# Kernel tuning notes

Hardware: AMD Instinct MI355X
Metric: run time of the kernel (lower is better)

The kernel has to match this reference:

```python
import jax, jax.numpy as jnp
import numpy as np

N, K, BINS, DIM = 32, 16, 100, 2
LAST_TIME = 1.0
PRIOR_LAMBDA = 1.0e5
T_INIT, T_LAST = 1.0, 2.0
JITTER = 1e-5
EPS = 1e-12


def _b_kernel(t1, t2, ls, x0_c):
    """RBF kernel between train bin centers t2 (rows) and query times t1 (cols),
    with an independent x0 block prepended (block_diag). Returns (len(t2)+1, len(t1)+1)."""
    tm = t1[None, :] - t2[:, None]                      # (P, M)
    ker = jnp.exp(-0.5 * (tm / ls[0]) ** 2)
    P, M = ker.shape
    top = jnp.concatenate([x0_c ** 2, jnp.zeros((M,), ker.dtype)])[None, :]   # (1, M+1)
    bot = jnp.concatenate([jnp.zeros((P, 1), ker.dtype), ker], axis=1)        # (P, M+1)
    return jnp.concatenate([top, bot], axis=0)


def setup_inputs() -> dict:
    key = jax.random.key(0)
    ks = jax.random.split(key, 7)
    return {
        "x0": jax.random.normal(ks[0], (N, DIM), jnp.float32),
        "v": 0.1 * jax.random.normal(ks[1], (BINS, N, DIM), jnp.float32),
        "beta": jax.random.normal(ks[2], (N,), jnp.float32),
        "prior_sigma": 0.1 + 0.9 * jax.random.uniform(ks[3], (1,), jnp.float32),
        "prior_B_x0_c": 0.5 + jax.random.uniform(ks[4], (1,), jnp.float32),
        "prior_B_ls": 0.1 + 0.4 * jax.random.uniform(ks[5], (1,), jnp.float32),
        "prior_C_Q": 0.1 * jax.random.normal(ks[6], (N, K), jnp.float32),
        "sample_size": 100,
    }


def reference(x0, v, beta, prior_sigma, prior_B_x0_c, prior_B_ls, prior_C_Q, sample_size):
    bounds = jnp.linspace(0.0, LAST_TIME, BINS + 1)
    centers = 0.5 * (bounds[1:] + bounds[:-1])           # (BINS,)

    # ---- __compute_inv_train_cov (Woodbury via Kronecker factors) ----
    Bk = _b_kernel(centers, centers, prior_B_ls, prior_B_x0_c)          # (BINS+1, BINS+1)
    B_factor = jnp.linalg.cholesky(Bk + JITTER * jnp.eye(BINS + 1, dtype=Bk.dtype))
    C_factor = prior_C_Q                                                 # (N, K)
    D_factor = jnp.eye(DIM, dtype=x0.dtype)

    sigma_sq = jnp.clip(prior_sigma, 5.0 / BINS, None)[0] ** 2
    sigma_sq_inv = 1.0 / sigma_sq
    lambda_sq = PRIOR_LAMBDA ** 2
    reduced_dim = K * (BINS + 1) * DIM
    final_dim = N * (BINS + 1) * DIM

    R = jnp.eye(reduced_dim, dtype=x0.dtype) + sigma_sq_inv * jnp.kron(
        B_factor.T @ B_factor, jnp.kron(C_factor.T @ C_factor, D_factor.T @ D_factor))
    R_factor = jnp.linalg.cholesky(R)
    R_factor_inv = jnp.linalg.inv(R_factor).T
    K_factor = jnp.kron(B_factor, jnp.kron(C_factor, D_factor))          # (final_dim, reduced_dim)
    f = sigma_sq_inv * (K_factor @ R_factor_inv)
    inv_train_cov = (1.0 / lambda_sq) * (sigma_sq_inv * jnp.eye(final_dim, dtype=x0.dtype) - f @ f.T)

    # ---- get_v_pred / get_x_pred (noise term omitted for determinism) ----
    ts = jnp.linspace(T_INIT, T_LAST, sample_size)[:-1]                  # (T,)
    delta_t = ts[1] - ts[0]
    T = sample_size - 1

    B_cross = _b_kernel(ts, centers, prior_B_ls, prior_B_x0_c)[:, 1:]    # (BINS+1, T)
    CCt = C_factor @ C_factor.T                                          # (N, N)
    test_train_cov = lambda_sq * jnp.kron(B_cross, jnp.kron(CCt, D_factor @ D_factor.T))  # (final_dim, T*N*DIM)

    x0v = jnp.concatenate([x0.reshape(-1), v.reshape(-1)])               # (final_dim,)
    pred_v = ((test_train_cov.T @ inv_train_cov) @ x0v).reshape(T, N, DIM)

    bin_width = LAST_TIME / BINS
    x_last = x0 + bin_width * v.sum(axis=0)                              # (N, DIM)
    xt = x_last[None] + (ts - LAST_TIME)[:, None, None] * pred_v         # (T, N, DIM)

    # ---- intensity integral ----
    beta_mat = beta[:, None] + beta[None, :]                             # (N, N)
    sq = jnp.sum((xt[:, :, None, :] - xt[:, None, :, :]) ** 2, axis=-1)  # (T, N, N)
    dist = jnp.sqrt(jnp.maximum(sq, EPS))
    lambda_pred = jnp.sum(jnp.exp(beta_mat[None] - dist), axis=0) * delta_t
    return lambda_pred
```

## Files before the change

kernel.cpp:

```cpp
#include <hip/hip_runtime.h>
#include <math.h>

#define NBINS 100
#define NN    32
#define KD    16
#define NT    99

#define OFF_H   0
#define OFF_QT  3200
#define OFF_XL  3712

template<int CTRL>
__device__ __forceinline__ float fmov_dpp(float x) {
  return __int_as_float(
      __builtin_amdgcn_update_dpp(0, __float_as_int(x), CTRL, 0xf, 0xf, true));
}
__device__ __forceinline__ float frdlane(float x, int lane) {
  return __int_as_float(__builtin_amdgcn_readlane(__float_as_int(x), lane));
}
__device__ __forceinline__ float fshup(float x, float c0, int lane) {
  float v = fmov_dpp<0x111>(x);
  float x15 = frdlane(x, 15), x31 = frdlane(x, 31), x47 = frdlane(x, 47);
  v = (lane == 0)  ? c0  : v;
  v = (lane == 16) ? x15 : v;
  v = (lane == 32) ? x31 : v;
  v = (lane == 48) ? x47 : v;
  return v;
}
__device__ __forceinline__ float frdpos(float lo, float hi, int k) {
  return (k < 64) ? frdlane(lo, k) : frdlane(hi, k - 64);
}
__device__ __forceinline__ float frcp(float x) {
  float r = __builtin_amdgcn_rcpf(x);
  return r * (2.0f - x * r);
}

#define RD_LO(lo, hi, idx)  frdlane(lo, idx)
#define RD_MIX(lo, hi, idx) frdpos(lo, hi, ((idx) <= 99 ? (idx) : 99))

#define FWD_STEP(RD)                                                     \
  {                                                                      \
    float iuk = frcp(uk);                                                \
    Lrow[l * 101 + k] = u_lo * iuk;                                      \
    if (hiv) Lrow[ahi * 101 + k] = u_hi * iuk;                           \
    float dk = P * iuk * iuk;                                            \
    sdl = (l == k)   ? dk : sdl;                                         \
    sdh = (ahi == k) ? dk : sdh;                                         \
    float a0 = r0k * iuk, a1 = r1k * iuk;                                \
    float r0k1 = RD(r0_lo, r0_hi, k + 1);                                \
    float r1k1 = RD(r1_lo, r1_hi, k + 1);                                \
    float uk2  = RD(u_lo, u_hi, k + 2);                                  \
    float vk3  = RD(v_lo, v_hi, k + 3);                                  \
    if (l > k)   { r0_lo -= a0 * u_lo; r1_lo -= a1 * u_lo; }             \
    if (ahi > k) { r0_hi -= a0 * u_hi; r1_hi -= a1 * u_hi; }             \
    r0k = r0k1 - a0 * uk1;                                               \
    r1k = r1k1 - a1 * uk1;                                               \
    float g = vk1 * iuk;                                                 \
    float u63 = frdlane(u_lo, 63);                                       \
    float u1_lo = fshup(u_lo, 0.0f, l);                                  \
    float u1_hi = fshup(u_hi, u63, l);                                   \
    u_lo = u1_lo - g * v_lo;  u_hi = u1_hi - g * v_hi;                   \
    v_lo = v_lo - g * u1_lo;  v_hi = v_hi - g * u1_hi;                   \
    P *= (1.0f - g * g);                                                 \
    float uk_n  = uk  - g * vk1;                                         \
    float uk1_n = uk1 - g * vk2;                                         \
    float vk1_n = vk2 - g * uk1;                                         \
    float vk2_n = vk3 - g * uk2;                                         \
    uk = uk_n; uk1 = uk1_n; vk1 = vk1_n; vk2 = vk2_n;                    \
  }

__global__ __launch_bounds__(64) void k1_all(
    const float* __restrict__ x0, const float* __restrict__ v_in,
    const float* __restrict__ sigma_in, const float* __restrict__ ls_in,
    const float* __restrict__ Cq, float* __restrict__ ws)
{
  extern __shared__ float fsm[];
  float* Lrow  = fsm;
  float* vT    = Lrow + 100 * 101;
  float* QTl   = vT + 64 * 101;
  __shared__ float A[16 * 17], Vv[16 * 17];
  __shared__ float csC[16], csS[16];
  __shared__ float CqS[NN * KD];

  const int l = threadIdx.x;
  const int j = blockIdx.x;
  const int r = l >> 2, c0 = l & 3;
  const float ls = ls_in[0];
  const float i2 = -0.5f / (ls * ls);
  float sig = fmaxf(sigma_in[0], 0.05f);
  const double sinvd = 1.0 / ((double)sig * (double)sig);
  const float sinvf = (float)sinvd;
  const int ahi = 64 + l;
  const bool hiv = (ahi < 100);

  for (int p = 0; p < NBINS; ++p) vT[l * 101 + p] = v_in[p * 64 + l];
  for (int e = l; e < NN * KD; e += 64) CqS[e] = Cq[e];

  if (j == 0) {
    float acc = 0.f;
    for (int p = 0; p < NBINS; ++p) acc += vT[l * 101 + p];
    ws[OFF_XL + l] = x0[l] + 0.01f * acc;
  }

  #pragma unroll
  for (int k = 0; k < 4; ++k) {
    int ci = c0 + 4 * k;
    float acc = 0.f;
    for (int n = 0; n < NN; ++n)
      acc += CqS[n * 16 + r] * CqS[n * 16 + ci];
    A[r * 17 + ci] = acc;
    Vv[r * 17 + ci] = (r == ci) ? 1.0f : 0.0f;
  }

  for (int sweep = 0; sweep < 4; ++sweep)
  for (int m = 1; m <= 15; ++m) {
    const int hb = 31 - __clz(m);
    const int lowm = (1 << hb) - 1;
    if (l < 8) {
      int p = ((l & ~lowm) << 1) | (l & lowm), q = p ^ m;
      float app = A[p * 17 + p], aqq = A[q * 17 + q], apq = A[p * 17 + q];
      float c = 1.0f, s = 0.0f;
      if (fabsf(apq) > 1e-30f) {
        float th = (aqq - app) * 0.5f * __builtin_amdgcn_rcpf(apq);
        float t_ = __builtin_amdgcn_rcpf(fabsf(th) + sqrtf(th * th + 1.0f));
        t_ = (th >= 0.0f) ? t_ : -t_;
        c = __builtin_amdgcn_rsqf(t_ * t_ + 1.0f);
        s = t_ * c;
      }
      csC[p] = c; csS[p] = -s;
      csC[q] = c; csS[q] = s;
    }
    const int rh = r ^ m;
    float ar = csC[r], br = csS[r];
    float nA[4], nV[4];
    #pragma unroll
    for (int k = 0; k < 4; ++k) {
      int ci = c0 + 4 * k, ch = ci ^ m;
      float ac = csC[ci], bc = csS[ci];
      float a_rc = A[r * 17 + ci],  a_hc = A[rh * 17 + ci];
      float a_rh = A[r * 17 + ch],  a_hh = A[rh * 17 + ch];
      float v_rc = Vv[r * 17 + ci], v_rh = Vv[r * 17 + ch];
      nA[k] = ac * (ar * a_rc + br * a_hc) + bc * (ar * a_rh + br * a_hh);
      nV[k] = ac * v_rc + bc * v_rh;
    }
    #pragma unroll
    for (int k = 0; k < 4; ++k) {
      int ci = c0 + 4 * k;
      A[r * 17 + ci] = nA[k];
      Vv[r * 17 + ci] = nV[k];
    }
  }

  float muj = A[j * 17 + j];
  if (muj < 0.f) muj = 0.f;
  const float c = (float)(sinvd * (double)muj);
  if (j == 0) {
    for (int e = l; e < 512; e += 64) {
      int jq = e >> 5, n = e & 31;
      float acc = 0.f;
      for (int k2 = 0; k2 < 16; ++k2)
        acc += CqS[n * 16 + k2] * Vv[k2 * 17 + jq];
      QTl[e] = acc;
      ws[OFF_QT + e] = acc;
    }
  } else if (l < 32) {
    float acc = 0.f;
    for (int k2 = 0; k2 < 16; ++k2)
      acc += CqS[l * 16 + k2] * Vv[k2 * 17 + j];
    QTl[j * 32 + l] = acc;
  }

  float s0l = 0.f, s1l = 0.f, s0h = 0.f, s1h = 0.f;
  for (int n = 0; n < NN; ++n) {
    float qv = QTl[j * 32 + n];
    s0l += qv * vT[(2 * n) * 101 + l];
    s1l += qv * vT[(2 * n + 1) * 101 + l];
    if (hiv) {
      s0h += qv * vT[(2 * n) * 101 + ahi];
      s1h += qv * vT[(2 * n + 1) * 101 + ahi];
    }
  }

  const float m0  = 1.0f + c * (1.0f + 1e-5f);
  const float im0 = frcp(m0);
  float gl = expf((0.01f * (float)l) * (0.01f * (float)l) * i2);
  float gh = expf((0.01f * (float)ahi) * (0.01f * (float)ahi) * i2);
  float u_lo = (l == 0) ? 1.0f : c * gl * im0;
  float u_hi = hiv ? c * gh * im0 : 0.0f;
  float v_lo = (l == 0) ? 0.0f : u_lo;
  float v_hi = u_hi;
  float r0_lo = s0l * im0, r1_lo = s1l * im0;
  float r0_hi = hiv ? s0h * im0 : 0.0f;
  float r1_hi = hiv ? s1h * im0 : 0.0f;
  float P = 1.0f;
  float sdl = 0.f, sdh = 0.f;

  float uk  = frdlane(u_lo, 0);
  float uk1 = frdlane(u_lo, 1);
  float vk1 = frdlane(v_lo, 1);
  float vk2 = frdlane(v_lo, 2);
  float r0k = frdlane(r0_lo, 0);
  float r1k = frdlane(r1_lo, 0);

  for (int k = 0; k < 60; ++k)  FWD_STEP(RD_LO)
  for (int k = 60; k < 99; ++k) FWD_STEP(RD_MIX)
  {
    const int k = 99;
    float iuk = frcp(uk);
    Lrow[l * 101 + k] = u_lo * iuk;
    if (hiv) Lrow[ahi * 101 + k] = u_hi * iuk;
    float dk = P * iuk * iuk;
    sdh = (ahi == k) ? dk : sdh;
  }

  float x0_lo = r0_lo * sdl, x1_lo = r1_lo * sdl;
  float x0_hi = r0_hi * sdh, x1_hi = r1_hi * sdh;

  float Ll = Lrow[99 * 101 + l];
  float Lh = hiv ? Lrow[99 * 101 + ahi] : 0.0f;
  for (int k = 99; k >= 1; --k) {
    float nLl = Lrow[(k - 1) * 101 + l];
    float nLh = hiv ? Lrow[(k - 1) * 101 + ahi] : 0.0f;
    float xk0 = frdpos(x0_lo, x0_hi, k);
    float xk1 = frdpos(x1_lo, x1_hi, k);
    if (l < k)   { x0_lo -= xk0 * Ll; x1_lo -= xk1 * Ll; }
    if (ahi < k) { x0_hi -= xk0 * Lh; x1_hi -= xk1 * Lh; }
    Ll = nLl; Lh = nLh;
  }

  ws[OFF_H + l * 32 + j * 2 + 0] = sinvf * x0_lo;
  ws[OFF_H + l * 32 + j * 2 + 1] = sinvf * x1_lo;
  if (hiv) {
    ws[OFF_H + ahi * 32 + j * 2 + 0] = sinvf * x0_hi;
    ws[OFF_H + ahi * 32 + j * 2 + 1] = sinvf * x1_hi;
  }
}

#define L_H   0
#define L_QT  3200
#define L_XL  3712
#define L_BC  3776
#define L_Z   13676
#define L_XT  16844
#define L_PS  23180
#define L_TOT 23436

__global__ __launch_bounds__(256) void k_tail(
    const float* __restrict__ ls_in, const float* __restrict__ beta,
    const float* __restrict__ ws, float* __restrict__ out)
{
  extern __shared__ float lds[];
  const int tid = threadIdx.x;
  const float ls = ls_in[0];
  const float i2 = -0.5f / (ls * ls);

  for (int e = tid; e < 3200; e += 256) lds[L_H + e] = ws[OFF_H + e];
  for (int e = tid; e < 512; e += 256)  lds[L_QT + e] = ws[OFF_QT + e];
  if (tid < 64) lds[L_XL + tid] = ws[OFF_XL + tid];
  for (int e = tid; e < NT * NBINS; e += 256) {
    int t = e / NBINS, p = e - t * NBINS;
    float tst = 1.0f + (float)t * (1.0f / 99.0f);
    float dd = tst - ((float)p + 0.5f) * 0.01f;
    lds[L_BC + e] = expf(dd * dd * i2);
  }
  __syncthreads();

  for (int dot = tid; dot < NT * 32; dot += 256) {
    int t = dot >> 5, jd = dot & 31;
    float acc = 0.f;
    for (int p = 0; p < NBINS; ++p)
      acc += lds[L_BC + t * NBINS + p] * lds[L_H + p * 32 + jd];
    lds[L_Z + dot] = acc;
  }
  __syncthreads();

  for (int e = tid; e < NT * 64; e += 256) {
    int t = e >> 6, nd = e & 63, n = nd >> 1, d = nd & 1;
    float acc = 0.f;
    for (int jq = 0; jq < 16; ++jq)
      acc += lds[L_QT + jq * 32 + n] * lds[L_Z + t * 32 + jq * 2 + d];
    float trel = (float)t * (1.0f / 99.0f);
    lds[L_XT + e] = lds[L_XL + nd] + trel * acc;
  }
  __syncthreads();

  {
    const int pl = tid & 63, tc = tid >> 6;
    const int gp = blockIdx.x * 64 + pl;
    const int i = gp >> 5, jj = gp & 31;
    const float bsum = beta[i] + beta[jj];
    const int t0 = tc * 25, t1 = (t0 + 25 < NT) ? t0 + 25 : NT;
    float acc = 0.f;
    for (int t = t0; t < t1; ++t) {
      float2 xi = *(const float2*)&lds[L_XT + t * 64 + 2 * i];
      float2 xj = *(const float2*)&lds[L_XT + t * 64 + 2 * jj];
      float dx = xi.x - xj.x, dy = xi.y - xj.y;
      float sq = fmaxf(dx * dx + dy * dy, 1e-12f);
      acc += expf(bsum - sqrtf(sq));
    }
    lds[L_PS + tc * 64 + pl] = acc;
  }
  __syncthreads();
  if (tid < 64) {
    float s = lds[L_PS + tid] + lds[L_PS + 64 + tid]
            + lds[L_PS + 128 + tid] + lds[L_PS + 192 + tid];
    out[blockIdx.x * 64 + tid] = s * (1.0f / 99.0f);
  }
}

extern "C" void kernel_launch(void* const* d_in, const int* in_sizes, int n_in,
                              void* d_out, int out_size, void* d_ws, size_t ws_size,
                              hipStream_t stream) {
  const float* x0    = (const float*)d_in[0];
  const float* v     = (const float*)d_in[1];
  const float* beta  = (const float*)d_in[2];
  const float* sigma = (const float*)d_in[3];
  const float* ls    = (const float*)d_in[5];
  const float* Cq    = (const float*)d_in[6];
  float* out = (float*)d_out;
  float* ws  = (float*)d_ws;

  const size_t smem1 = (size_t)(100 * 101 + 64 * 101 + 512) * sizeof(float);
  k1_all<<<16, 64, smem1, stream>>>(x0, v, sigma, ls, Cq, ws);
  k_tail<<<16, 256, (size_t)L_TOT * sizeof(float), stream>>>(ls, beta, ws, out);
}
```

Measured before the change: 101.5 us.

## Overlap v transpose load with Jacobi eigensolve using a second wavefront

```diff
diff --git a/kernel.cpp b/kernel.cpp
--- a/kernel.cpp
+++ b/kernel.cpp
@@ -69,7 +69,7 @@
     uk = uk_n; uk1 = uk1_n; vk1 = vk1_n; vk2 = vk2_n;                    \
   }
 
-__global__ __launch_bounds__(64) void k1_all(
+__global__ __launch_bounds__(128) void k1_all(
     const float* __restrict__ x0, const float* __restrict__ v_in,
     const float* __restrict__ sigma_in, const float* __restrict__ ls_in,
     const float* __restrict__ Cq, float* __restrict__ ws)
@@ -79,10 +79,11 @@
   float* vT    = Lrow + 100 * 101;
   float* QTl   = vT + 64 * 101;
   __shared__ float A[16 * 17], Vv[16 * 17];
-  __shared__ float csC[16], csS[16];
   __shared__ float CqS[NN * KD];
 
-  const int l = threadIdx.x;
+  const int tid = threadIdx.x;
+  const int l = tid & 63;
+  const int wv = tid >> 6;
   const int j = blockIdx.x;
   const int r = l >> 2, c0 = l & 3;
   const float ls = ls_in[0];
@@ -93,82 +94,96 @@
   const int ahi = 64 + l;
   const bool hiv = (ahi < 100);
 
-  for (int p = 0; p < NBINS; ++p) vT[l * 101 + p] = v_in[p * 64 + l];
-  for (int e = l; e < NN * KD; e += 64) CqS[e] = Cq[e];
-
-  if (j == 0) {
-    float acc = 0.f;
-    for (int p = 0; p < NBINS; ++p) acc += vT[l * 101 + p];
-    ws[OFF_XL + l] = x0[l] + 0.01f * acc;
-  }
-
-  #pragma unroll
-  for (int k = 0; k < 4; ++k) {
-    int ci = c0 + 4 * k;
-    float acc = 0.f;
-    for (int n = 0; n < NN; ++n)
-      acc += CqS[n * 16 + r] * CqS[n * 16 + ci];
-    A[r * 17 + ci] = acc;
-    Vv[r * 17 + ci] = (r == ci) ? 1.0f : 0.0f;
-  }
-
-  for (int sweep = 0; sweep < 4; ++sweep)
-  for (int m = 1; m <= 15; ++m) {
-    const int hb = 31 - __clz(m);
-    const int lowm = (1 << hb) - 1;
-    if (l < 8) {
-      int p = ((l & ~lowm) << 1) | (l & lowm), q = p ^ m;
-      float app = A[p * 17 + p], aqq = A[q * 17 + q], apq = A[p * 17 + q];
-      float c = 1.0f, s = 0.0f;
-      if (fabsf(apq) > 1e-30f) {
-        float th = (aqq - app) * 0.5f * __builtin_amdgcn_rcpf(apq);
-        float t_ = __builtin_amdgcn_rcpf(fabsf(th) + sqrtf(th * th + 1.0f));
-        t_ = (th >= 0.0f) ? t_ : -t_;
-        c = __builtin_amdgcn_rsqf(t_ * t_ + 1.0f);
-        s = t_ * c;
-      }
-      csC[p] = c; csS[p] = -s;
-      csC[q] = c; csS[q] = s;
-    }
-    const int rh = r ^ m;
-    float ar = csC[r], br = csS[r];
-    float nA[4], nV[4];
-    #pragma unroll
-    for (int k = 0; k < 4; ++k) {
-      int ci = c0 + 4 * k, ch = ci ^ m;
-      float ac = csC[ci], bc = csS[ci];
-      float a_rc = A[r * 17 + ci],  a_hc = A[rh * 17 + ci];
-      float a_rh = A[r * 17 + ch],  a_hh = A[rh * 17 + ch];
-      float v_rc = Vv[r * 17 + ci], v_rh = Vv[r * 17 + ch];
-      nA[k] = ac * (ar * a_rc + br * a_hc) + bc * (ar * a_rh + br * a_hh);
-      nV[k] = ac * v_rc + bc * v_rh;
-    }
+  float c = 0.0f;
+
+  if (wv == 1) {
+    for (int p = 0; p < NBINS; ++p) vT[l * 101 + p] = v_in[p * 64 + l];
+    if (j == 0) {
+      float acc = 0.f;
+      for (int p = 0; p < NBINS; ++p) acc += vT[l * 101 + p];
+      ws[OFF_XL + l] = x0[l] + 0.01f * acc;
+    }
+  } else {
+    for (int e = l; e < NN * KD; e += 64) CqS[e] = Cq[e];
     #pragma unroll
     for (int k = 0; k < 4; ++k) {
       int ci = c0 + 4 * k;
-      A[r * 17 + ci] = nA[k];
-      Vv[r * 17 + ci] = nV[k];
-    }
-  }
-
-  float muj = A[j * 17 + j];
-  if (muj < 0.f) muj = 0.f;
-  const float c = (float)(sinvd * (double)muj);
-  if (j == 0) {
-    for (int e = l; e < 512; e += 64) {
-      int jq = e >> 5, n = e & 31;
+      float acc = 0.f;
+      for (int n = 0; n < NN; ++n)
+        acc += CqS[n * 16 + r] * CqS[n * 16 + ci];
+      A[r * 17 + ci] = acc;
+      Vv[r * 17 + ci] = (r == ci) ? 1.0f : 0.0f;
+    }
+
+    for (int sweep = 0; sweep < 4; ++sweep)
+    for (int m = 1; m <= 15; ++m) {
+      const int hb = 31 - __clz(m);
+      const int lowm = (1 << hb) - 1;
+      float cc_ = 1.0f, ss_ = 0.0f;
+      if (l < 8) {
+        int p = ((l & ~lowm) << 1) | (l & lowm), q = p ^ m;
+        float app = A[p * 17 + p], aqq = A[q * 17 + q], apq = A[p * 17 + q];
+        if (fabsf(apq) > 1e-30f) {
+          float th = (aqq - app) * 0.5f * __builtin_amdgcn_rcpf(apq);
+          float t_ = __builtin_amdgcn_rcpf(fabsf(th) + sqrtf(th * th + 1.0f));
+          t_ = (th >= 0.0f) ? t_ : -t_;
+          cc_ = __builtin_amdgcn_rsqf(t_ * t_ + 1.0f);
+          ss_ = t_ * cc_;
+        }
+      }
+      int hibr = (r >> hb) & 1;
+      int pr = hibr ? (r ^ m) : r;
+      int idr = ((pr >> (hb + 1)) << hb) | (pr & lowm);
+      float ar = __shfl(cc_, idr, 64);
+      float sr = __shfl(ss_, idr, 64);
+      float br = hibr ? sr : -sr;
+      const int rh = r ^ m;
+      float nA[4], nV[4];
+      #pragma unroll
+      for (int k = 0; k < 4; ++k) {
+        int ci = c0 + 4 * k, ch = ci ^ m;
+        int hibc = (ci >> hb) & 1;
+        int pc = hibc ? (ci ^ m) : ci;
+        int idc = ((pc >> (hb + 1)) << hb) | (pc & lowm);
+        float ac = __shfl(cc_, idc, 64);
+        float sc = __shfl(ss_, idc, 64);
+        float bc = hibc ? sc : -sc;
+        float a_rc = A[r * 17 + ci],  a_hc = A[rh * 17 + ci];
+        float a_rh = A[r * 17 + ch],  a_hh = A[rh * 17 + ch];
+        float v_rc = Vv[r * 17 + ci], v_rh = Vv[r * 17 + ch];
+        nA[k] = ac * (ar * a_rc + br * a_hc) + bc * (ar * a_rh + br * a_hh);
+        nV[k] = ac * v_rc + bc * v_rh;
+      }
+      #pragma unroll
+      for (int k = 0; k < 4; ++k) {
+        int ci = c0 + 4 * k;
+        A[r * 17 + ci] = nA[k];
+        Vv[r * 17 + ci] = nV[k];
+      }
+    }
+
+    float muj = A[j * 17 + j];
+    if (muj < 0.f) muj = 0.f;
+    c = (float)(sinvd * (double)muj);
+    if (j == 0) {
+      for (int e = l; e < 512; e += 64) {
+        int jq = e >> 5, n = e & 31;
+        float acc = 0.f;
+        for (int k2 = 0; k2 < 16; ++k2)
+          acc += CqS[n * 16 + k2] * Vv[k2 * 17 + jq];
+        QTl[e] = acc;
+        ws[OFF_QT + e] = acc;
+      }
+    } else if (l < 32) {
       float acc = 0.f;
       for (int k2 = 0; k2 < 16; ++k2)
-        acc += CqS[n * 16 + k2] * Vv[k2 * 17 + jq];
-      QTl[e] = acc;
-      ws[OFF_QT + e] = acc;
-    }
-  } else if (l < 32) {
-    float acc = 0.f;
-    for (int k2 = 0; k2 < 16; ++k2)
-      acc += CqS[l * 16 + k2] * Vv[k2 * 17 + j];
-    QTl[j * 32 + l] = acc;
-  }
+        acc += CqS[l * 16 + k2] * Vv[k2 * 17 + j];
+      QTl[j * 32 + l] = acc;
+    }
+  }
+
+  __syncthreads();
+  if (wv == 1) return;
 
   float s0l = 0.f, s1l = 0.f, s0h = 0.f, s1h = 0.f;
   for (int n = 0; n < NN; ++n) {
@@ -321,6 +336,6 @@
   float* ws  = (float*)d_ws;
 
   const size_t smem1 = (size_t)(100 * 101 + 64 * 101 + 512) * sizeof(float);
-  k1_all<<<16, 64, smem1, stream>>>(x0, v, sigma, ls, Cq, ws);
+  k1_all<<<16, 128, smem1, stream>>>(x0, v, sigma, ls, Cq, ws);
   k_tail<<<16, 256, (size_t)L_TOT * sizeof(float), stream>>>(ls, beta, ws, out);
 }
```

Measured after the change: 107.2 us. 1.06x slower.
